# Kernel tuning notes

Measured on AMD Instinct MI355X. Metric: run time of the kernel, lower is better.

## Reference

```python
import jax, jax.numpy as jnp
import numpy as np

D_MODEL, H, D_FF = 1024, 16, 4096
B, S = 2, 2048
EPS = 1e-6


def setup_inputs() -> dict:
    key = jax.random.key(0)
    ks = jax.random.split(key, 12)
    sc = 0.02
    p = lambda k, shape: (jax.random.normal(k, shape, dtype=jnp.float32) * sc)
    return {
        "x": jax.random.normal(ks[0], (B, S, D_MODEL), dtype=jnp.float32),
        "mask": jnp.ones((B, 1, 1, S), dtype=jnp.int32),
        "wq": p(ks[1], (D_MODEL, D_MODEL)), "bq": jnp.zeros((D_MODEL,), jnp.float32),
        "wk": p(ks[2], (D_MODEL, D_MODEL)), "bk": jnp.zeros((D_MODEL,), jnp.float32),
        "wv": p(ks[3], (D_MODEL, D_MODEL)), "bv": jnp.zeros((D_MODEL,), jnp.float32),
        "wo": p(ks[4], (D_MODEL, D_MODEL)), "bo": jnp.zeros((D_MODEL,), jnp.float32),
        "w1": p(ks[5], (D_FF, D_MODEL)), "b1": jnp.zeros((D_FF,), jnp.float32),
        "w2": p(ks[6], (D_MODEL, D_FF)), "b2": jnp.zeros((D_MODEL,), jnp.float32),
        "ln1_a": jnp.ones((D_MODEL,), jnp.float32), "ln1_b": jnp.zeros((D_MODEL,), jnp.float32),
        "ln2_a": jnp.ones((D_MODEL,), jnp.float32), "ln2_b": jnp.zeros((D_MODEL,), jnp.float32),
    }


def _layernorm(x, alpha, beta):
    # Matches the torch module: unbiased std (ddof=1), eps added to std (not var).
    mean = jnp.mean(x, axis=-1, keepdims=True)
    std = jnp.std(x, axis=-1, keepdims=True, ddof=1)
    return alpha * (x - mean) / (std + EPS) + beta


def _mha(x, mask, wq, bq, wk, bk, wv, bv, wo, bo):
    b, s, d = x.shape
    d_k = d // H
    # torch Linear: y = x @ W^T + b
    q = (x @ wq.T + bq).reshape(b, s, H, d_k).transpose(0, 2, 1, 3)
    k = (x @ wk.T + bk).reshape(b, s, H, d_k).transpose(0, 2, 1, 3)
    v = (x @ wv.T + bv).reshape(b, s, H, d_k).transpose(0, 2, 1, 3)
    scores = jnp.einsum("bhqd,bhkd->bhqk", q, k) / jnp.sqrt(jnp.float32(d_k))
    scores = jnp.where(mask == 0, jnp.float32(-1e9), scores)
    attn = jax.nn.softmax(scores, axis=-1)
    out = jnp.einsum("bhqk,bhkd->bhqd", attn, v)
    out = out.transpose(0, 2, 1, 3).reshape(b, s, d)
    return out @ wo.T + bo


def reference(x, mask, wq, bq, wk, bk, wv, bv, wo, bo, w1, b1, w2, b2,
              ln1_a, ln1_b, ln2_a, ln2_b):
    # Pre-LN MHA + residual
    h1 = _layernorm(x, ln1_a, ln1_b)
    x = x + _mha(h1, mask, wq, bq, wk, bk, wv, bv, wo, bo)
    # Pre-LN FFN + residual (dropout=0 -> identity)
    h2 = _layernorm(x, ln2_a, ln2_b)
    ff = jax.nn.relu(h2 @ w1.T + b1) @ w2.T + b2
    return x + ff
```

## Files before the change

### kernel.cpp

```cpp
#include <hip/hip_runtime.h>
#include <cstdint>
#include <cstddef>

typedef short bf16x8 __attribute__((ext_vector_type(8)));
typedef short bf16x4 __attribute__((ext_vector_type(4)));
typedef float f32x4 __attribute__((ext_vector_type(4)));

#define D_MODEL 1024
#define SEQ     2048
#define NBATCH  2
#define NH      16
#define DKH     64
#define DFF     4096
#define MROWS   (NBATCH * SEQ)

#if __has_builtin(__builtin_amdgcn_mfma_f32_16x16x16bf16_1k)
#define HAVE_MFMA16 1
#define MFMA16(a, b, c) __builtin_amdgcn_mfma_f32_16x16x16bf16_1k(a, b, c, 0, 0, 0)
#elif __has_builtin(__builtin_amdgcn_mfma_f32_16x16x16_bf16)
#define HAVE_MFMA16 1
#define MFMA16(a, b, c) __builtin_amdgcn_mfma_f32_16x16x16_bf16(a, b, c, 0, 0, 0)
#else
#define HAVE_MFMA16 0
#endif

__device__ __forceinline__ unsigned short f2bf(float f) {
  unsigned u = __builtin_bit_cast(unsigned, f);
  u += 0x7fffu + ((u >> 16) & 1u);
  return (unsigned short)(u >> 16);
}
__device__ __forceinline__ unsigned packbf2(float lo, float hi) {
  unsigned r;
  asm("v_cvt_pk_bf16_f32 %0, %1, %2" : "=v"(r) : "v"(lo), "v"(hi));
  return r;
}
__device__ __forceinline__ void gload_lds16(const void* g, void* l) {
  __builtin_amdgcn_global_load_lds(
      (const __attribute__((address_space(1))) unsigned*)g,
      (__attribute__((address_space(3))) unsigned*)l, 16, 0, 0);
}

__global__ __launch_bounds__(256) void cast_weights_kernel(
    const float* __restrict__ wq, const float* __restrict__ wk,
    const float* __restrict__ wv, const float* __restrict__ wo,
    const float* __restrict__ w1, const float* __restrict__ w2,
    const int* __restrict__ mask, unsigned short* __restrict__ dst,
    float* __restrict__ maskf) {
  const int TOT4 = (12 << 20) >> 2;
  const int gid = blockIdx.x * blockDim.x + threadIdx.x;
  for (int i4 = gid; i4 < TOT4; i4 += gridDim.x * blockDim.x) {
    int i = i4 << 2;
    const float* src;
    int off;
    if (i < (4 << 20)) {
      src = (i < (2 << 20)) ? ((i < (1 << 20)) ? wq : wk)
                            : ((i < (3 << 20)) ? wv : wo);
      off = i & ((1 << 20) - 1);
    } else if (i < (8 << 20)) { src = w1; off = i - (4 << 20); }
    else                      { src = w2; off = i - (8 << 20); }
    float4 v = *(const float4*)(src + off);
    ushort4 o;
    o.x = f2bf(v.x); o.y = f2bf(v.y); o.z = f2bf(v.z); o.w = f2bf(v.w);
    *(ushort4*)(dst + i) = o;
  }
  if (gid < (NBATCH * SEQ / 4)) {
    int4 m = ((const int4*)mask)[gid];
    float4 f;
    f.x = (m.x == 0) ? -1e9f : 0.f;
    f.y = (m.y == 0) ? -1e9f : 0.f;
    f.z = (m.z == 0) ? -1e9f : 0.f;
    f.w = (m.w == 0) ? -1e9f : 0.f;
    ((float4*)maskf)[gid] = f;
  }
}

__global__ __launch_bounds__(256) void ln_kernel(
    const float* __restrict__ x, const float* __restrict__ alpha,
    const float* __restrict__ beta, unsigned short* __restrict__ out) {
  const int row = blockIdx.x;
  const int t = threadIdx.x;
  float4 v = *(const float4*)(x + (size_t)row * D_MODEL + t * 4);
  float s = v.x + v.y + v.z + v.w;
#pragma unroll
  for (int o = 1; o < 64; o <<= 1) s += __shfl_xor(s, o, 64);
  __shared__ float red[8];
  if ((t & 63) == 0) red[t >> 6] = s;
  __syncthreads();
  float mean = (red[0] + red[1] + red[2] + red[3]) * (1.f / D_MODEL);
  float dx = v.x - mean, dy = v.y - mean, dz = v.z - mean, dw = v.w - mean;
  float sq = dx * dx + dy * dy + dz * dz + dw * dw;
#pragma unroll
  for (int o = 1; o < 64; o <<= 1) sq += __shfl_xor(sq, o, 64);
  if ((t & 63) == 0) red[4 + (t >> 6)] = sq;
  __syncthreads();
  float var = (red[4] + red[5] + red[6] + red[7]) * (1.f / (D_MODEL - 1));
  float inv = 1.f / (sqrtf(var) + 1e-6f);
  float4 a = *(const float4*)(alpha + t * 4);
  float4 be = *(const float4*)(beta + t * 4);
  ushort4 o4;
  o4.x = f2bf(a.x * dx * inv + be.x);
  o4.y = f2bf(a.y * dy * inv + be.y);
  o4.z = f2bf(a.z * dz * inv + be.z);
  o4.w = f2bf(a.w * dw * inv + be.w);
  *(ushort4*)(out + (size_t)row * D_MODEL + t * 4) = o4;
}

#define GEMM_STAGE(A_, W_, LD_, koff_, kt_, buf_)                                  \
  {                                                                                \
    int ke_ = (koff_) + (kt_) * 32;                                                \
    gload_lds16(A_ + (size_t)(m0 + srow) * (LD_) + ke_ + sce, &lds[(buf_)][0][t * 8]);        \
    gload_lds16(A_ + (size_t)(m0 + 64 + srow) * (LD_) + ke_ + sce, &lds[(buf_)][0][2048 + t * 8]); \
    gload_lds16(W_ + (size_t)(n0 + srow) * (LD_) + ke_ + sce, &lds[(buf_)][1][t * 8]);        \
    gload_lds16(W_ + (size_t)(n0 + 64 + srow) * (LD_) + ke_ + sce, &lds[(buf_)][1][2048 + t * 8]); \
  }

#define GEMM_MAINLOOP(A_, W_, LD_, K_, koff_)                                      \
  GEMM_STAGE(A_, W_, LD_, koff_, 0, 0);                                            \
  for (int kt = 0; kt < ((K_) >> 5); ++kt) {                                       \
    __syncthreads();                                                               \
    if (kt + 1 < ((K_) >> 5)) GEMM_STAGE(A_, W_, LD_, koff_, kt + 1, (kt + 1) & 1); \
    const unsigned short* la = lds[kt & 1][0];                                     \
    const unsigned short* lb = lds[kt & 1][1];                                     \
    bf16x8 af[4], bfr[4];                                                          \
    _Pragma("unroll") for (int i = 0; i < 4; i++) {                                \
      af[i]  = *(const bf16x8*)&la[(wm + i * 16 + c) * 32 + g * 8];                \
      bfr[i] = *(const bf16x8*)&lb[(wn + i * 16 + c) * 32 + g * 8];                \
    }                                                                              \
    _Pragma("unroll") for (int mi = 0; mi < 4; mi++)                               \
      _Pragma("unroll") for (int ni = 0; ni < 4; ni++)                             \
        acc[mi][ni] = __builtin_amdgcn_mfma_f32_16x16x32_bf16(af[mi], bfr[ni],     \
                                                              acc[mi][ni], 0, 0, 0); \
  }

enum { MODE_BF16 = 0, MODE_RELU = 2, MODE_PARTIAL = 4 };

template <int MODE>
__global__ __launch_bounds__(256) void gemm_bt(
    const unsigned short* __restrict__ A, const unsigned short* __restrict__ W,
    const float* __restrict__ bias, void* __restrict__ outp, int M, int N, int K) {
  __shared__ unsigned short lds[2][2][128 * 32];
  const int t = threadIdx.x;
  const int lane = t & 63, wid = t >> 6;
  const int g = lane >> 4, c = lane & 15;
  const int m0 = blockIdx.y * 128, n0 = blockIdx.x * 128;
  const int wm = (wid >> 1) * 64, wn = (wid & 1) * 64;
  const int srow = t >> 2, sce = (t & 3) * 8;
  const int ldk = K * gridDim.z;
  const int koff = blockIdx.z * K;

  f32x4 zero = {0.f, 0.f, 0.f, 0.f};
  f32x4 acc[4][4];
#pragma unroll
  for (int i = 0; i < 4; i++)
#pragma unroll
    for (int j = 0; j < 4; j++) acc[i][j] = zero;

  GEMM_MAINLOOP(A, W, ldk, K, koff);

  float bv[4];
#pragma unroll
  for (int ni = 0; ni < 4; ni++)
    bv[ni] = (MODE == MODE_PARTIAL) ? 0.f : bias[n0 + wn + ni * 16 + c];

  float* po = (MODE == MODE_PARTIAL)
                  ? ((float*)outp + (size_t)blockIdx.z * M * N) : (float*)outp;

#pragma unroll
  for (int mi = 0; mi < 4; mi++) {
#pragma unroll
    for (int ni = 0; ni < 4; ni++) {
      const int mb = m0 + wm + mi * 16 + g * 4;
      const int n = n0 + wn + ni * 16 + c;
#pragma unroll
      for (int r = 0; r < 4; r++) {
        const int m = mb + r;
        float v = acc[mi][ni][r] + bv[ni];
        if (MODE == MODE_RELU) v = fmaxf(v, 0.f);
        if (MODE == MODE_PARTIAL) {
          po[(size_t)m * N + n] = v;
        } else {
          ((unsigned short*)outp)[(size_t)m * N + n] = f2bf(v);
        }
      }
    }
  }
}

__global__ __launch_bounds__(256) void gemm_qkv(
    const unsigned short* __restrict__ A, const unsigned short* __restrict__ Wbase,
    const float* __restrict__ bq, const float* __restrict__ bk,
    const float* __restrict__ bv_, unsigned short* __restrict__ qkout,
    unsigned short* __restrict__ vtout) {
  __shared__ unsigned short lds[2][2][128 * 32];
  const int t = threadIdx.x;
  const int lane = t & 63, wid = t >> 6;
  const int g = lane >> 4, c = lane & 15;
  const int wsel = blockIdx.x >> 3;
  const int m0 = blockIdx.y * 128, n0 = (blockIdx.x & 7) * 128;
  const int wm = (wid >> 1) * 64, wn = (wid & 1) * 64;
  const int srow = t >> 2, sce = (t & 3) * 8;
  const unsigned short* W = Wbase + ((size_t)wsel << 20);
  const float* bias = (wsel == 0) ? bq : (wsel == 1) ? bk : bv_;

  f32x4 zero = {0.f, 0.f, 0.f, 0.f};
  f32x4 acc[4][4];
#pragma unroll
  for (int i = 0; i < 4; i++)
#pragma unroll
    for (int j = 0; j < 4; j++) acc[i][j] = zero;

  GEMM_MAINLOOP(A, W, 1024, 1024, 0);

  float bvv[4];
#pragma unroll
  for (int ni = 0; ni < 4; ni++) bvv[ni] = bias[n0 + wn + ni * 16 + c];
  const float qsc = (wsel == 0) ? 0.125f : 1.f;

  if (wsel < 2) {
    unsigned short* outp = qkout + ((size_t)wsel << 22);
#pragma unroll
    for (int mi = 0; mi < 4; mi++) {
#pragma unroll
      for (int ni = 0; ni < 4; ni++) {
        const int mb = m0 + wm + mi * 16 + g * 4;
        const int n = n0 + wn + ni * 16 + c;
#pragma unroll
        for (int r = 0; r < 4; r++)
          outp[(size_t)(mb + r) * 1024 + n] = f2bf((acc[mi][ni][r] + bvv[ni]) * qsc);
      }
    }
  } else {
#pragma unroll
    for (int mi = 0; mi < 4; mi++) {
#pragma unroll
      for (int ni = 0; ni < 4; ni++) {
        const int mb = m0 + wm + mi * 16 + g * 4;
        const int n = n0 + wn + ni * 16 + c;
        const int b = mb >> 11, s2 = mb & 2047;
        ushort4 o4;
        o4.x = f2bf(acc[mi][ni][0] + bvv[ni]);
        o4.y = f2bf(acc[mi][ni][1] + bvv[ni]);
        o4.z = f2bf(acc[mi][ni][2] + bvv[ni]);
        o4.w = f2bf(acc[mi][ni][3] + bvv[ni]);
        *(ushort4*)(vtout + ((size_t)(b * 1024 + n)) * 2048 + s2) = o4;
      }
    }
  }
}

#define ATTN_STAGE(base_, buf_)                                                     \
  {                                                                                 \
    const int i0 = t, i1 = t + 128;                                                 \
    gload_lds16(Kb + (size_t)((base_) + (i0 >> 3)) * D_MODEL +                      \
                    (((i0 & 7) ^ ((i0 >> 3) & 7)) << 3), &Klds[buf_][i0 * 8]);      \
    gload_lds16(Kb + (size_t)((base_) + (i1 >> 3)) * D_MODEL +                      \
                    (((i1 & 7) ^ ((i1 >> 3) & 7)) << 3), &Klds[buf_][i1 * 8]);      \
    gload_lds16(Vb + (size_t)(i0 >> 2) * SEQ + (base_) +                            \
                    (((i0 & 3) ^ ((i0 >> 2) & 3)) << 3), &Vlds[buf_][i0 * 8]);      \
    gload_lds16(Vb + (size_t)(i1 >> 2) * SEQ + (base_) +                            \
                    (((i1 & 3) ^ ((i1 >> 2) & 3)) << 3), &Vlds[buf_][i1 * 8]);      \
  }

__global__ __launch_bounds__(128, 4) void attn_kernel(
    const unsigned short* __restrict__ Q, const unsigned short* __restrict__ Kmat,
    const unsigned short* __restrict__ Vt, const float* __restrict__ maskf,
    unsigned short* __restrict__ O) {
  __shared__ unsigned short Klds[2][32 * 64];
  __shared__ unsigned short Vlds[2][64 * 32];
  const int t = threadIdx.x, lane = t & 63, wid = t >> 6;
  const int g = lane >> 4, c = lane & 15;
  const int qt = blockIdx.x, bh = blockIdx.y;
  const int b = bh >> 4, h = bh & 15;
  const int q0 = qt * 32 + wid * 16;

  const unsigned short* Qb = Q + (size_t)b * SEQ * D_MODEL + h * DKH;
  const unsigned short* Kb = Kmat + (size_t)b * SEQ * D_MODEL + h * DKH;
  const unsigned short* Vb = Vt + (size_t)bh * DKH * SEQ;
  const float* mbf = maskf + b * SEQ;

  bf16x8 qf[2];
#pragma unroll
  for (int kd = 0; kd < 2; kd++)
    qf[kd] = *(const bf16x8*)&Qb[(size_t)(q0 + c) * D_MODEL + kd * 32 + g * 8];

  f32x4 zero = {0.f, 0.f, 0.f, 0.f};
  f32x4 of[4];
#pragma unroll
  for (int j = 0; j < 4; j++) of[j] = zero;
  float mrun = -1e30f, lrun = 0.f;

  ATTN_STAGE(0, 0);

  for (int kv = 0; kv < 64; ++kv) {
    const int buf = kv & 1;
    const int base = kv * 32;
    __syncthreads();
    if (kv < 63) ATTN_STAGE(base + 32, buf ^ 1);

    bf16x8 kf[4];
#pragma unroll
    for (int nb = 0; nb < 2; nb++)
#pragma unroll
      for (int kd = 0; kd < 2; kd++)
        kf[nb * 2 + kd] = *(const bf16x8*)&Klds[buf][(nb * 16 + c) * 64 +
                                                     (((kd * 4 + g) ^ (c & 7)) << 3)];
#if HAVE_MFMA16
    bf16x4 vv[2][4];
#pragma unroll
    for (int nb = 0; nb < 2; nb++)
#pragma unroll
      for (int dkb = 0; dkb < 4; dkb++) {
        const int vrow = dkb * 16 + c;
        const int vbyte = vrow * 64 + ((((nb << 1) + (g >> 1)) ^ (c & 3)) << 4) +
                          ((g & 1) << 3);
        vv[nb][dkb] = *(const bf16x4*)((const char*)Vlds[buf] + vbyte);
      }
#else
    bf16x8 vf[4];
#pragma unroll
    for (int dkb = 0; dkb < 4; dkb++)
      vf[dkb] = *(const bf16x8*)&Vlds[buf][(dkb * 16 + c) * 32 +
                                           ((g ^ (c & 3)) << 3)];
#endif

    float4 ma0 = *(const float4*)&mbf[base + g * 4];
    float4 ma1 = *(const float4*)&mbf[base + 16 + g * 4];

    f32x4 sf[2];
#pragma unroll
    for (int nb = 0; nb < 2; nb++) {
      f32x4 s = zero;
      s = __builtin_amdgcn_mfma_f32_16x16x32_bf16(kf[nb * 2 + 0], qf[0], s, 0, 0, 0);
      s = __builtin_amdgcn_mfma_f32_16x16x32_bf16(kf[nb * 2 + 1], qf[1], s, 0, 0, 0);
      sf[nb] = s;
    }

    sf[0][0] += ma0.x; sf[0][1] += ma0.y; sf[0][2] += ma0.z; sf[0][3] += ma0.w;
    sf[1][0] += ma1.x; sf[1][1] += ma1.y; sf[1][2] += ma1.z; sf[1][3] += ma1.w;

    float pm = fmaxf(fmaxf(fmaxf(sf[0][0], sf[0][1]), fmaxf(sf[0][2], sf[0][3])),
                     fmaxf(fmaxf(sf[1][0], sf[1][1]), fmaxf(sf[1][2], sf[1][3])));
    pm = fmaxf(pm, __shfl_xor(pm, 16, 64));
    pm = fmaxf(pm, __shfl_xor(pm, 32, 64));
    if (!__all(pm <= mrun + 8.f)) {
      float mnew = fmaxf(mrun, pm);
      float fsc = exp2f((mrun - mnew) * 1.44269504f);
      lrun *= fsc;
#pragma unroll
      for (int dkb = 0; dkb < 4; dkb++) of[dkb] *= fsc;
      mrun = mnew;
    }
    const float mb2 = mrun * 1.44269504f;
    float ps = 0.f;
#pragma unroll
    for (int nb = 0; nb < 2; nb++)
#pragma unroll
      for (int r = 0; r < 4; r++) {
        float p = exp2f(fmaf(sf[nb][r], 1.44269504f, -mb2));
        sf[nb][r] = p;
        ps += p;
      }
    lrun += ps;

#if HAVE_MFMA16
#pragma unroll
    for (int nb = 0; nb < 2; nb++) {
      unsigned plo = packbf2(sf[nb][0], sf[nb][1]);
      unsigned phi = packbf2(sf[nb][2], sf[nb][3]);
      unsigned long long uu = (unsigned long long)plo |
                              ((unsigned long long)phi << 32);
      bf16x4 pf = __builtin_bit_cast(bf16x4, uu);
#pragma unroll
      for (int dkb = 0; dkb < 4; dkb++)
        of[dkb] = MFMA16(vv[nb][dkb], pf, of[dkb]);
    }
#else
    unsigned pk00 = packbf2(sf[0][0], sf[0][1]);
    unsigned pk01 = packbf2(sf[0][2], sf[0][3]);
    unsigned pk10 = packbf2(sf[1][0], sf[1][1]);
    unsigned pk11 = packbf2(sf[1][2], sf[1][3]);
    const int la = ((g & 1) << 5) + c;
    const int lb2 = la + 16;
    unsigned a00 = __shfl(pk00, la, 64), a01 = __shfl(pk01, la, 64);
    unsigned a10 = __shfl(pk10, la, 64), a11 = __shfl(pk11, la, 64);
    unsigned b00 = __shfl(pk00, lb2, 64), b01 = __shfl(pk01, lb2, 64);
    unsigned b10 = __shfl(pk10, lb2, 64), b11 = __shfl(pk11, lb2, 64);
    const bool hi2 = (g >= 2);
    uint4 pw;
    pw.x = hi2 ? a10 : a00;
    pw.y = hi2 ? a11 : a01;
    pw.z = hi2 ? b10 : b00;
    pw.w = hi2 ? b11 : b01;
    bf16x8 pf = __builtin_bit_cast(bf16x8, pw);
#pragma unroll
    for (int dkb = 0; dkb < 4; dkb++)
      of[dkb] = __builtin_amdgcn_mfma_f32_16x16x32_bf16(vf[dkb], pf, of[dkb], 0, 0, 0);
#endif
  }

  float lt = lrun;
  lt += __shfl_xor(lt, 16, 64);
  lt += __shfl_xor(lt, 32, 64);
  float inv = 1.f / lt;
#pragma unroll
  for (int dkb = 0; dkb < 4; dkb++) {
    ushort4 o4;
    o4.x = f2bf(of[dkb][0] * inv);
    o4.y = f2bf(of[dkb][1] * inv);
    o4.z = f2bf(of[dkb][2] * inv);
    o4.w = f2bf(of[dkb][3] * inv);
    *(ushort4*)&O[(size_t)(b * SEQ + q0 + c) * D_MODEL + h * DKH + dkb * 16 +
                  g * 4] = o4;
  }
}

__global__ __launch_bounds__(256) void proj_ln2_kernel(
    const float* __restrict__ x, const float* __restrict__ P0,
    const float* __restrict__ P1, const float* __restrict__ bo,
    const float* __restrict__ alpha, const float* __restrict__ beta,
    float* __restrict__ x2, unsigned short* __restrict__ h2) {
  const int row = blockIdx.x;
  const int t = threadIdx.x;
  const size_t idx = (size_t)row * D_MODEL + t * 4;
  float4 xv = *(const float4*)(x + idx);
  float4 p0 = *(const float4*)(P0 + idx);
  float4 p1 = *(const float4*)(P1 + idx);
  float4 bo4 = *(const float4*)(bo + t * 4);
  float4 v;
  v.x = xv.x + p0.x + p1.x + bo4.x;
  v.y = xv.y + p0.y + p1.y + bo4.y;
  v.z = xv.z + p0.z + p1.z + bo4.z;
  v.w = xv.w + p0.w + p1.w + bo4.w;
  *(float4*)(x2 + idx) = v;

  float s = v.x + v.y + v.z + v.w;
#pragma unroll
  for (int o = 1; o < 64; o <<= 1) s += __shfl_xor(s, o, 64);
  __shared__ float red[8];
  if ((t & 63) == 0) red[t >> 6] = s;
  __syncthreads();
  float mean = (red[0] + red[1] + red[2] + red[3]) * (1.f / D_MODEL);
  float dx = v.x - mean, dy = v.y - mean, dz = v.z - mean, dw = v.w - mean;
  float sq = dx * dx + dy * dy + dz * dz + dw * dw;
#pragma unroll
  for (int o = 1; o < 64; o <<= 1) sq += __shfl_xor(sq, o, 64);
  if ((t & 63) == 0) red[4 + (t >> 6)] = sq;
  __syncthreads();
  float var = (red[4] + red[5] + red[6] + red[7]) * (1.f / (D_MODEL - 1));
  float inv = 1.f / (sqrtf(var) + 1e-6f);
  float4 a = *(const float4*)(alpha + t * 4);
  float4 be = *(const float4*)(beta + t * 4);
  ushort4 o4;
  o4.x = f2bf(a.x * dx * inv + be.x);
  o4.y = f2bf(a.y * dy * inv + be.y);
  o4.z = f2bf(a.z * dz * inv + be.z);
  o4.w = f2bf(a.w * dw * inv + be.w);
  *(ushort4*)(h2 + idx) = o4;
}

__global__ __launch_bounds__(256) void ffn2_add_kernel(
    const float* __restrict__ x2, const float* __restrict__ Q0,
    const float* __restrict__ Q1, const float* __restrict__ b2,
    float* __restrict__ out) {
  const int i4 = blockIdx.x * blockDim.x + threadIdx.x;
  const size_t idx = (size_t)i4 * 4;
  float4 a = *(const float4*)(x2 + idx);
  float4 q0 = *(const float4*)(Q0 + idx);
  float4 q1 = *(const float4*)(Q1 + idx);
  float4 b = *(const float4*)(b2 + ((i4 & 255) * 4));
  float4 v;
  v.x = a.x + q0.x + q1.x + b.x;
  v.y = a.y + q0.y + q1.y + b.y;
  v.z = a.z + q0.z + q1.z + b.z;
  v.w = a.w + q0.w + q1.w + b.w;
  *(float4*)(out + idx) = v;
}

extern "C" void kernel_launch(void* const* d_in, const int* in_sizes, int n_in,
                              void* d_out, int out_size, void* d_ws, size_t ws_size,
                              hipStream_t stream) {
  (void)in_sizes; (void)n_in; (void)out_size; (void)ws_size;
  const float* x    = (const float*)d_in[0];
  const int*   mask = (const int*)d_in[1];
  const float* wq   = (const float*)d_in[2];
  const float* bq   = (const float*)d_in[3];
  const float* wk   = (const float*)d_in[4];
  const float* bk   = (const float*)d_in[5];
  const float* wv   = (const float*)d_in[6];
  const float* bv   = (const float*)d_in[7];
  const float* wo   = (const float*)d_in[8];
  const float* bo   = (const float*)d_in[9];
  const float* w1   = (const float*)d_in[10];
  const float* b1   = (const float*)d_in[11];
  const float* w2   = (const float*)d_in[12];
  const float* b2   = (const float*)d_in[13];
  const float* ln1a = (const float*)d_in[14];
  const float* ln1b = (const float*)d_in[15];
  const float* ln2a = (const float*)d_in[16];
  const float* ln2b = (const float*)d_in[17];

  char* ws = (char*)d_ws;
  unsigned short* w_bf  = (unsigned short*)ws;
  unsigned short* wq_bf = w_bf;
  unsigned short* wo_bf = w_bf + (3u << 20);
  unsigned short* w1_bf = w_bf + (4u << 20);
  unsigned short* w2_bf = w_bf + (8u << 20);
  unsigned short* h1    = (unsigned short*)(ws + (24u << 20));
  unsigned short* qbuf  = (unsigned short*)(ws + (32u << 20));
  unsigned short* kbuf  = (unsigned short*)(ws + (40u << 20));
  unsigned short* vtbuf = (unsigned short*)(ws + (48u << 20));
  unsigned short* attnb = (unsigned short*)(ws + (56u << 20));
  float*          x2    = (float*)(ws + (64u << 20));
  unsigned short* h2    = (unsigned short*)(ws + (80u << 20));
  unsigned short* ffn1  = (unsigned short*)(ws + (88u << 20));
  float*          pp    = (float*)(ws + (88u << 20));
  float*          qq    = (float*)(ws + (24u << 20));
  float*          maskf = (float*)(ws + (120u << 20));

  cast_weights_kernel<<<1024, 256, 0, stream>>>(wq, wk, wv, wo, w1, w2, mask,
                                                w_bf, maskf);
  ln_kernel<<<MROWS, 256, 0, stream>>>(x, ln1a, ln1b, h1);
  gemm_qkv<<<dim3(24, 32), 256, 0, stream>>>(h1, wq_bf, bq, bk, bv, qbuf, vtbuf);
  attn_kernel<<<dim3(64, 32), 128, 0, stream>>>(qbuf, kbuf, vtbuf, maskf, attnb);
  gemm_bt<MODE_PARTIAL><<<dim3(8, 32, 2), 256, 0, stream>>>(
      attnb, wo_bf, nullptr, (void*)pp, MROWS, D_MODEL, 512);
  proj_ln2_kernel<<<MROWS, 256, 0, stream>>>(
      x, pp, pp + (size_t)MROWS * D_MODEL, bo, ln2a, ln2b, x2, h2);
  gemm_bt<MODE_RELU><<<dim3(32, 32), 256, 0, stream>>>(
      h2, w1_bf, b1, (void*)ffn1, MROWS, DFF, D_MODEL);
  gemm_bt<MODE_PARTIAL><<<dim3(8, 32, 2), 256, 0, stream>>>(
      ffn1, w2_bf, nullptr, (void*)qq, MROWS, D_MODEL, 2048);
  ffn2_add_kernel<<<4096, 256, 0, stream>>>(
      x2, qq, qq + (size_t)MROWS * D_MODEL, b2, (float*)d_out);
}
```

Baseline: 295.9 us.

## Triple-buffer attention K/V loads with 256-thread blocks and LDS-resident mask

The attention kernel moves to 256-thread blocks covering 64 query rows, with each thread issuing one K and one V async load per stage. It switches from double to triple buffering, using a vmcnt wait plus a raw s_barrier so loads stay in flight two iterations ahead. The mask row is preloaded into LDS once instead of being read from global memory every iteration, and s_setprio brackets the MFMA sections. The aim is to hide global-load latency and cut per-iteration sync and mask traffic, at the cost of more LDS per block and fewer blocks in the grid.

```diff
diff --git a/kernel.cpp b/kernel.cpp
--- a/kernel.cpp
+++ b/kernel.cpp
@@ -248,30 +248,26 @@
   }
 }
 
-#define ATTN_STAGE(base_, buf_)                                                     \
+#define ATTN_STAGE3(base_, buf_)                                                    \
   {                                                                                 \
-    const int i0 = t, i1 = t + 128;                                                 \
-    gload_lds16(Kb + (size_t)((base_) + (i0 >> 3)) * D_MODEL +                      \
-                    (((i0 & 7) ^ ((i0 >> 3) & 7)) << 3), &Klds[buf_][i0 * 8]);      \
-    gload_lds16(Kb + (size_t)((base_) + (i1 >> 3)) * D_MODEL +                      \
-                    (((i1 & 7) ^ ((i1 >> 3) & 7)) << 3), &Klds[buf_][i1 * 8]);      \
-    gload_lds16(Vb + (size_t)(i0 >> 2) * SEQ + (base_) +                            \
-                    (((i0 & 3) ^ ((i0 >> 2) & 3)) << 3), &Vlds[buf_][i0 * 8]);      \
-    gload_lds16(Vb + (size_t)(i1 >> 2) * SEQ + (base_) +                            \
-                    (((i1 & 3) ^ ((i1 >> 2) & 3)) << 3), &Vlds[buf_][i1 * 8]);      \
-  }
-
-__global__ __launch_bounds__(128, 4) void attn_kernel(
+    gload_lds16(Kb + (size_t)((base_) + (t >> 3)) * D_MODEL +                       \
+                    (((t & 7) ^ ((t >> 3) & 7)) << 3), &Klds[buf_][t * 8]);         \
+    gload_lds16(Vb + (size_t)(t >> 2) * SEQ + (base_) +                             \
+                    (((t & 3) ^ ((t >> 2) & 3)) << 3), &Vlds[buf_][t * 8]);         \
+  }
+
+__global__ __launch_bounds__(256, 4) void attn_kernel(
     const unsigned short* __restrict__ Q, const unsigned short* __restrict__ Kmat,
     const unsigned short* __restrict__ Vt, const float* __restrict__ maskf,
     unsigned short* __restrict__ O) {
-  __shared__ unsigned short Klds[2][32 * 64];
-  __shared__ unsigned short Vlds[2][64 * 32];
+  __shared__ unsigned short Klds[3][32 * 64];
+  __shared__ unsigned short Vlds[3][64 * 32];
+  __shared__ float masklds[SEQ];
   const int t = threadIdx.x, lane = t & 63, wid = t >> 6;
   const int g = lane >> 4, c = lane & 15;
   const int qt = blockIdx.x, bh = blockIdx.y;
   const int b = bh >> 4, h = bh & 15;
-  const int q0 = qt * 32 + wid * 16;
+  const int q0 = qt * 64 + wid * 16;
 
   const unsigned short* Qb = Q + (size_t)b * SEQ * D_MODEL + h * DKH;
   const unsigned short* Kb = Kmat + (size_t)b * SEQ * D_MODEL + h * DKH;
@@ -289,13 +285,25 @@
   for (int j = 0; j < 4; j++) of[j] = zero;
   float mrun = -1e30f, lrun = 0.f;
 
-  ATTN_STAGE(0, 0);
+  {
+    const int mo = wid * 256 + lane * 4;
+    gload_lds16(mbf + mo, &masklds[mo]);
+    gload_lds16(mbf + 1024 + mo, &masklds[1024 + mo]);
+  }
+  ATTN_STAGE3(0, 0);
+  ATTN_STAGE3(32, 1);
 
   for (int kv = 0; kv < 64; ++kv) {
-    const int buf = kv & 1;
+    const int buf = kv % 3;
     const int base = kv * 32;
-    __syncthreads();
-    if (kv < 63) ATTN_STAGE(base + 32, buf ^ 1);
+    asm volatile("s_waitcnt vmcnt(2)" ::: "memory");
+    __builtin_amdgcn_sched_barrier(0);
+    __builtin_amdgcn_s_barrier();
+    __builtin_amdgcn_sched_barrier(0);
+    if (kv < 62) {
+      const int nbuf = (kv + 2) % 3;
+      ATTN_STAGE3(base + 64, nbuf);
+    }
 
     bf16x8 kf[4];
 #pragma unroll
@@ -323,10 +331,11 @@
                                            ((g ^ (c & 3)) << 3)];
 #endif
 
-    float4 ma0 = *(const float4*)&mbf[base + g * 4];
-    float4 ma1 = *(const float4*)&mbf[base + 16 + g * 4];
+    float4 ma0 = *(const float4*)&masklds[base + g * 4];
+    float4 ma1 = *(const float4*)&masklds[base + 16 + g * 4];
 
     f32x4 sf[2];
+    __builtin_amdgcn_s_setprio(1);
 #pragma unroll
     for (int nb = 0; nb < 2; nb++) {
       f32x4 s = zero;
@@ -334,6 +343,7 @@
       s = __builtin_amdgcn_mfma_f32_16x16x32_bf16(kf[nb * 2 + 1], qf[1], s, 0, 0, 0);
       sf[nb] = s;
     }
+    __builtin_amdgcn_s_setprio(0);
 
     sf[0][0] += ma0.x; sf[0][1] += ma0.y; sf[0][2] += ma0.z; sf[0][3] += ma0.w;
     sf[1][0] += ma1.x; sf[1][1] += ma1.y; sf[1][2] += ma1.z; sf[1][3] += ma1.w;
@@ -370,9 +380,11 @@
       unsigned long long uu = (unsigned long long)plo |
                               ((unsigned long long)phi << 32);
       bf16x4 pf = __builtin_bit_cast(bf16x4, uu);
+      __builtin_amdgcn_s_setprio(1);
 #pragma unroll
       for (int dkb = 0; dkb < 4; dkb++)
         of[dkb] = MFMA16(vv[nb][dkb], pf, of[dkb]);
+      __builtin_amdgcn_s_setprio(0);
     }
 #else
     unsigned pk00 = packbf2(sf[0][0], sf[0][1]);
@@ -521,7 +533,7 @@
                                                 w_bf, maskf);
   ln_kernel<<<MROWS, 256, 0, stream>>>(x, ln1a, ln1b, h1);
   gemm_qkv<<<dim3(24, 32), 256, 0, stream>>>(h1, wq_bf, bq, bk, bv, qbuf, vtbuf);
-  attn_kernel<<<dim3(64, 32), 128, 0, stream>>>(qbuf, kbuf, vtbuf, maskf, attnb);
+  attn_kernel<<<dim3(32, 32), 256, 0, stream>>>(qbuf, kbuf, vtbuf, maskf, attnb);
   gemm_bt<MODE_PARTIAL><<<dim3(8, 32, 2), 256, 0, stream>>>(
       attnb, wo_bf, nullptr, (void*)pp, MROWS, D_MODEL, 512);
   proj_ln2_kernel<<<MROWS, 256, 0, stream>>>(
```

After: 308.0 us. 4.1% more time.
